# Kernel optimization log

Measured on AMD Instinct MI355X. Metric: run time of the kernel, lower is better.

The kernel has to match this reference:

```python
import jax, jax.numpy as jnp
import numpy as np

B = 16384      # batch of samples
D = 65         # inps columns: 64 input spins + 1 output spin y
NA = 64        # auxiliary (threshold) spins
N = D + NA     # spins entering vspin expansion: 129
M = N + N * (N - 1) // 2  # degree-<=2 spin monomials: 8385
GAMMA = 1.0

# pairwise index pattern (i < j), computed once at trace time
_II, _JJ = np.triu_indices(N, k=1)


def batch_vspin(b):
    # b: [B, N] -> [B, N + N(N-1)/2]: linear terms then all pairwise products b_i*b_j (i<j)
    return jnp.concatenate([b, b[:, _II] * b[:, _JJ]], axis=-1)


def setup_inputs() -> dict:
    key = jax.random.key(0)
    k1, k2, k3, k4 = jax.random.split(key, 4)
    inps = jax.random.normal(k1, (B, D), dtype=jnp.float32)
    thresh_w = jax.random.normal(k2, (NA, D), dtype=jnp.float32) * 0.1
    thresh_b = jax.random.normal(k3, (NA,), dtype=jnp.float32) * 0.1
    main_w = jax.random.normal(k4, (1, M), dtype=jnp.float32) * 0.02
    return {"inps": inps, "thresh_w": thresh_w, "thresh_b": thresh_b, "main_w": main_w}


def reference(inps, thresh_w, thresh_b, main_w):
    inps = inps.astype(jnp.float32)
    x = inps[:, :-1]                      # [B, D-1]
    y = inps[:, -1:]                      # [B, 1]
    i_right = jnp.concatenate([x, y], axis=-1)    # [B, D]
    i_wrong = jnp.concatenate([x, -y], axis=-1)   # [B, D]

    w1 = i_right @ thresh_w.T + thresh_b          # [B, NA]
    w2 = i_wrong @ thresh_w.T + thresh_b          # [B, NA]
    t1 = jnp.tanh(GAMMA * w1)
    t2 = jnp.tanh(GAMMA * w2)

    b1 = jnp.concatenate([i_right, t1], axis=-1)  # [B, N]
    b2 = jnp.concatenate([i_wrong, t2], axis=-1)  # [B, N]
    v1 = batch_vspin(b1)                          # [B, M]
    v2 = batch_vspin(b2)                          # [B, M]

    diff = (v1 - v2) @ main_w.T + 1.0             # [B, 1]
    int_penalty = jnp.sum((GAMMA / 300.0) * ((1.0 - t1 ** 2) ** 2 + (1.0 - t2 ** 2) ** 2))
    neut_penalty = jnp.sum((t2 * w2 - t1 * w1) ** 2)
    return (diff, int_penalty, neut_penalty)
```

## Files before the change

### kernel.cpp

```cpp
#include <hip/hip_runtime.h>

#define B_SZ 16384
#define N_SP 129

typedef _Float16 half8 __attribute__((ext_vector_type(8)));
typedef float float4v __attribute__((ext_vector_type(4)));

#define WS_F32_BASE 6144
#define WS_TWY  (WS_F32_BASE)
#define WS_QXY  (WS_F32_BASE + 64)
#define WS_QYT  (WS_F32_BASE + 128)
#define WS_LINT (WS_F32_BASE + 192)
#define WS_LINY (WS_F32_BASE + 256)
#define WS_P1   (WS_F32_BASE + 320)
#define WS_P2   (WS_F32_BASE + 576)

__device__ __forceinline__ int qidx(int i, int j) {
  return N_SP + i * (2 * N_SP - i - 1) / 2 + (j - i - 1);
}

__device__ __forceinline__ float fast_tanh(float x) {
  float xc = fminf(fmaxf(x, -15.f), 15.f);
  float e = __expf(2.f * xc);
  return 1.f - 2.f / (e + 1.f);
}

__global__ void setup_kernel(const float* __restrict__ mw, const float* __restrict__ tw,
                             float* __restrict__ wsf) {
  int t = blockIdx.x * blockDim.x + threadIdx.x;
  if (t < 12288) {
    int frag = t >> 9;
    int e = t & 511;
    int lane = e >> 3, j = e & 7;
    int tbl = frag >> 3;
    int tg = frag & 7;
    int kt = tg >> 2, g = tg & 3;
    int k = kt * 32 + (lane >> 4) * 8 + j;
    int n = (lane & 15) + 16 * g;
    float v;
    if (tbl == 0) {
      v = tw[n * 65 + k];
    } else if (tbl == 1) {
      v = mw[qidx(n, 65 + k)];
    } else {
      v = 0.f;
      if (n != k) {
        int a = n < k ? n : k, b = n < k ? k : n;
        v = mw[qidx(65 + a, 65 + b)];
      }
    }
    ((_Float16*)wsf)[t] = (_Float16)v;
  } else if (t < 12352) {
    int u = t - 12288; wsf[WS_TWY + u] = tw[u * 65 + 64];
  } else if (t < 12416) {
    int i = t - 12352; wsf[WS_QXY + i] = mw[qidx(i, 64)];
  } else if (t < 12480) {
    int u = t - 12416; wsf[WS_QYT + u] = mw[qidx(64, 65 + u)];
  } else if (t < 12544) {
    int u = t - 12480; wsf[WS_LINT + u] = mw[65 + u];
  } else if (t == 12544) {
    wsf[WS_LINY] = mw[64];
  }
}

__global__ void main_kernel(const float* __restrict__ inps, const float* __restrict__ tb,
                            float* __restrict__ wsf, float* __restrict__ out) {
  __shared__ __align__(16) float s_x[4 * 1056];
  __shared__ __align__(16) float s_dt[4 * 1088];
  __shared__ float s_red[8];

  const int tid = threadIdx.x;
  const int l = tid & 63, wib = tid >> 6;
  const int wave = (blockIdx.x << 2) + wib;
  const int b0 = wave << 4;
  const int q = l >> 4, m = l & 15;

  float* xw = s_x + wib * 1056;
  float* dtw = s_dt + wib * 1088;

  const float* src = inps + b0 * 65;
#pragma unroll
  for (int t = 0; t < 16; t++) xw[t * 64 + l] = src[t * 64 + l];
  if (l < 16) xw[1024 + l] = src[1024 + l];

  const half8* fragh = (const half8*)wsf;

  float twyv[4], tbv[4], qxyv[4], qytv[4], lintv[4];
#pragma unroll
  for (int g = 0; g < 4; g++) {
    int u = m + 16 * g;
    twyv[g] = wsf[WS_TWY + u];
    tbv[g] = tb[u];
    qxyv[g] = wsf[WS_QXY + u];
    qytv[g] = wsf[WS_QYT + u];
    lintv[g] = wsf[WS_LINT + u];
  }
  const float liny = wsf[WS_LINY];

  half8 ax[2];
#pragma unroll
  for (int t = 0; t < 2; t++) {
    const float* xp = xw + m * 65 + t * 32 + q * 8;
#pragma unroll
    for (int j = 0; j < 8; j++) ax[t][j] = (_Float16)xp[j];
  }

  float4v acc[4];
#pragma unroll
  for (int g = 0; g < 4; g++) { acc[g][0] = 0.f; acc[g][1] = 0.f; acc[g][2] = 0.f; acc[g][3] = 0.f; }
#pragma unroll
  for (int g = 0; g < 4; g++)
#pragma unroll
    for (int t = 0; t < 2; t++)
      acc[g] = __builtin_amdgcn_mfma_f32_16x16x32_f16(ax[t], fragh[(t * 4 + g) * 64 + l], acc[g], 0, 0, 0);

  float yv[4];
#pragma unroll
  for (int r = 0; r < 4; r++) yv[r] = xw[(q * 4 + r) * 65 + 64];
  float dtv[4][4], stv[4][4];
  float pint = 0.f, pneut = 0.f;
#pragma unroll
  for (int g = 0; g < 4; g++)
#pragma unroll
    for (int r = 0; r < 4; r++) {
      float wpre = acc[g][r] + tbv[g];
      float w1 = wpre + twyv[g] * yv[r];
      float w2 = wpre - twyv[g] * yv[r];
      float t1 = fast_tanh(w1), t2 = fast_tanh(w2);
      float dt = t1 - t2, st = t1 + t2;
      dtv[g][r] = dt; stv[g][r] = st;
      float a1 = 1.f - t1 * t1, a2 = 1.f - t2 * t2;
      pint += a1 * a1 + a2 * a2;
      float nv = t2 * w2 - t1 * w1;
      pneut += nv * nv;
      dtw[(q * 4 + r) * 68 + m + 16 * g] = dt;
    }

  half8 adt[2];
#pragma unroll
  for (int t = 0; t < 2; t++) {
    const float* dp = dtw + m * 68 + t * 32 + q * 8;
#pragma unroll
    for (int j = 0; j < 8; j++) adt[t][j] = (_Float16)dp[j];
  }

  float4v rxt[4], rtt[4];
#pragma unroll
  for (int g = 0; g < 4; g++) {
    rxt[g][0] = 0.f; rxt[g][1] = 0.f; rxt[g][2] = 0.f; rxt[g][3] = 0.f;
    rtt[g][0] = 0.f; rtt[g][1] = 0.f; rtt[g][2] = 0.f; rtt[g][3] = 0.f;
  }
#pragma unroll
  for (int g = 0; g < 4; g++)
#pragma unroll
    for (int t = 0; t < 2; t++) {
      rxt[g] = __builtin_amdgcn_mfma_f32_16x16x32_f16(adt[t], fragh[(8 + t * 4 + g) * 64 + l], rxt[g], 0, 0, 0);
      rtt[g] = __builtin_amdgcn_mfma_f32_16x16x32_f16(adt[t], fragh[(16 + t * 4 + g) * 64 + l], rtt[g], 0, 0, 0);
    }

  float creg[4] = {0.f, 0.f, 0.f, 0.f};
#pragma unroll
  for (int g = 0; g < 4; g++)
#pragma unroll
    for (int r = 0; r < 4; r++) {
      float xv = xw[(q * 4 + r) * 65 + m + 16 * g];
      creg[r] += xv * (2.f * yv[r] * qxyv[g] + rxt[g][r])
               + yv[r] * stv[g][r] * qytv[g]
               + 0.5f * stv[g][r] * rtt[g][r]
               + lintv[g] * dtv[g][r];
    }
#pragma unroll
  for (int r = 0; r < 4; r++) {
    float c = creg[r];
    c += __shfl_xor(c, 1); c += __shfl_xor(c, 2);
    c += __shfl_xor(c, 4); c += __shfl_xor(c, 8);
    if (m == 0) out[b0 + q * 4 + r] = 1.f + 2.f * yv[r] * liny + c;
  }

#pragma unroll
  for (int off = 1; off < 64; off <<= 1) {
    pint += __shfl_xor(pint, off);
    pneut += __shfl_xor(pneut, off);
  }
  if (l == 0) { s_red[wib] = pint; s_red[4 + wib] = pneut; }
  __syncthreads();
  if (tid == 0) {
    wsf[WS_P1 + blockIdx.x] = s_red[0] + s_red[1] + s_red[2] + s_red[3];
    wsf[WS_P2 + blockIdx.x] = s_red[4] + s_red[5] + s_red[6] + s_red[7];
  }
}

__global__ __launch_bounds__(256) void reduce_kernel(const float* __restrict__ wsf,
                                                     float* __restrict__ out) {
  __shared__ float s[8];
  const int tid = threadIdx.x;
  float a = wsf[WS_P1 + tid];
  float b = wsf[WS_P2 + tid];
#pragma unroll
  for (int off = 1; off < 64; off <<= 1) {
    a += __shfl_xor(a, off);
    b += __shfl_xor(b, off);
  }
  const int w = tid >> 6, l = tid & 63;
  if (l == 0) { s[w] = a; s[4 + w] = b; }
  __syncthreads();
  if (tid == 0) {
    out[B_SZ] = (s[0] + s[1] + s[2] + s[3]) * (1.f / 300.f);
    out[B_SZ + 1] = s[4] + s[5] + s[6] + s[7];
  }
}

extern "C" void kernel_launch(void* const* d_in, const int* in_sizes, int n_in,
                              void* d_out, int out_size, void* d_ws, size_t ws_size,
                              hipStream_t stream) {
  const float* inps = (const float*)d_in[0];
  const float* tw   = (const float*)d_in[1];
  const float* tb   = (const float*)d_in[2];
  const float* mw   = (const float*)d_in[3];
  float* out = (float*)d_out;
  float* wsf = (float*)d_ws;
  setup_kernel<<<50, 256, 0, stream>>>(mw, tw, wsf);
  main_kernel<<<256, 256, 0, stream>>>(inps, tb, wsf, out);
  reduce_kernel<<<1, 256, 0, stream>>>(wsf, out);
}
```

Baseline: 73.25 us.

## Fuse weight-fragment setup into main kernel via shared memory and halve rows per wave

Removes the separate setup kernel: each block now gathers the fp16 weight fragments and the small per-spin tables straight into shared memory, which saves one launch and the global workspace round-trip. The grid is doubled to 512 blocks, with each wave handling 8 samples instead of 16, so half the MFMA output rows are idle and masked. Inputs are staged as fp16 in shared memory using float4 loads, which lets fragments be read with single vector loads. The cost is that every block repeats the 12K-element weight gather from global memory, and half of the MFMA work is wasted.

```diff
diff --git a/kernel.cpp b/kernel.cpp
--- a/kernel.cpp
+++ b/kernel.cpp
@@ -2,18 +2,14 @@
 
 #define B_SZ 16384
 #define N_SP 129
+#define GRID 512
+#define BLOCK 256
 
 typedef _Float16 half8 __attribute__((ext_vector_type(8)));
 typedef float float4v __attribute__((ext_vector_type(4)));
 
-#define WS_F32_BASE 6144
-#define WS_TWY  (WS_F32_BASE)
-#define WS_QXY  (WS_F32_BASE + 64)
-#define WS_QYT  (WS_F32_BASE + 128)
-#define WS_LINT (WS_F32_BASE + 192)
-#define WS_LINY (WS_F32_BASE + 256)
-#define WS_P1   (WS_F32_BASE + 320)
-#define WS_P2   (WS_F32_BASE + 576)
+#define WS_P1 0
+#define WS_P2 512
 
 __device__ __forceinline__ int qidx(int i, int j) {
   return N_SP + i * (2 * N_SP - i - 1) / 2 + (j - i - 1);
@@ -25,15 +21,24 @@
   return 1.f - 2.f / (e + 1.f);
 }
 
-__global__ void setup_kernel(const float* __restrict__ mw, const float* __restrict__ tw,
-                             float* __restrict__ wsf) {
-  int t = blockIdx.x * blockDim.x + threadIdx.x;
-  if (t < 12288) {
-    int frag = t >> 9;
-    int e = t & 511;
+__global__ __launch_bounds__(BLOCK, 2) void main_kernel(
+    const float* __restrict__ inps, const float* __restrict__ tw,
+    const float* __restrict__ tb, const float* __restrict__ mw,
+    float* __restrict__ out, float* __restrict__ wsf) {
+  __shared__ __align__(16) _Float16 s_frag[12288];
+  __shared__ __align__(16) _Float16 s_x[4 * 1152];
+  __shared__ __align__(16) _Float16 s_dt[4 * 1152];
+  __shared__ float s_small[324];
+  __shared__ float s_red[8];
+
+  const int tid = threadIdx.x;
+
+#pragma unroll 4
+  for (int s = 0; s < 48; s++) {
+    int idx = tid + BLOCK * s;
+    int frag = idx >> 9, e = idx & 511;
     int lane = e >> 3, j = e & 7;
-    int tbl = frag >> 3;
-    int tg = frag & 7;
+    int tbl = frag >> 3, tg = frag & 7;
     int kt = tg >> 2, g = tg & 3;
     int k = kt * 32 + (lane >> 4) * 8 + j;
     int n = (lane & 15) + 16 * g;
@@ -49,61 +54,70 @@
         v = mw[qidx(65 + a, 65 + b)];
       }
     }
-    ((_Float16*)wsf)[t] = (_Float16)v;
-  } else if (t < 12352) {
-    int u = t - 12288; wsf[WS_TWY + u] = tw[u * 65 + 64];
-  } else if (t < 12416) {
-    int i = t - 12352; wsf[WS_QXY + i] = mw[qidx(i, 64)];
-  } else if (t < 12480) {
-    int u = t - 12416; wsf[WS_QYT + u] = mw[qidx(64, 65 + u)];
-  } else if (t < 12544) {
-    int u = t - 12480; wsf[WS_LINT + u] = mw[65 + u];
-  } else if (t == 12544) {
-    wsf[WS_LINY] = mw[64];
-  }
-}
-
-__global__ void main_kernel(const float* __restrict__ inps, const float* __restrict__ tb,
-                            float* __restrict__ wsf, float* __restrict__ out) {
-  __shared__ __align__(16) float s_x[4 * 1056];
-  __shared__ __align__(16) float s_dt[4 * 1088];
-  __shared__ float s_red[8];
-
-  const int tid = threadIdx.x;
+    s_frag[idx] = (_Float16)v;
+  }
+  if (tid < 64) {
+    s_small[tid]       = tw[tid * 65 + 64];
+    s_small[64 + tid]  = mw[qidx(tid, 64)];
+    s_small[128 + tid] = mw[qidx(64, 65 + tid)];
+    s_small[192 + tid] = mw[65 + tid];
+    s_small[256 + tid] = tb[tid];
+  }
+  if (tid == 0) s_small[320] = mw[64];
+
   const int l = tid & 63, wib = tid >> 6;
   const int wave = (blockIdx.x << 2) + wib;
-  const int b0 = wave << 4;
+  const int b0 = wave << 3;
+  _Float16* xw = s_x + wib * 1152;
+  _Float16* dw = s_dt + wib * 1152;
+  {
+    const float4* src4 = (const float4*)(inps + b0 * 65);
+#pragma unroll
+    for (int it = 0; it < 2; it++) {
+      float4 v = src4[l + 64 * it];
+      const float* vp = (const float*)&v;
+      int f0 = (l + 64 * it) * 4;
+#pragma unroll
+      for (int c = 0; c < 4; c++) {
+        unsigned idx = f0 + c;
+        unsigned row = idx / 65u, col = idx - row * 65u;
+        xw[row * 72 + col] = (_Float16)vp[c];
+      }
+    }
+    if (l < 2) {
+      float4 v = src4[128 + l];
+      const float* vp = (const float*)&v;
+      int f0 = (128 + l) * 4;
+#pragma unroll
+      for (int c = 0; c < 4; c++) {
+        unsigned idx = f0 + c;
+        unsigned row = idx / 65u, col = idx - row * 65u;
+        xw[row * 72 + col] = (_Float16)vp[c];
+      }
+    }
+  }
+  __syncthreads();
+
   const int q = l >> 4, m = l & 15;
-
-  float* xw = s_x + wib * 1056;
-  float* dtw = s_dt + wib * 1088;
-
-  const float* src = inps + b0 * 65;
-#pragma unroll
-  for (int t = 0; t < 16; t++) xw[t * 64 + l] = src[t * 64 + l];
-  if (l < 16) xw[1024 + l] = src[1024 + l];
-
-  const half8* fragh = (const half8*)wsf;
+  const bool act = (q < 2);
 
   float twyv[4], tbv[4], qxyv[4], qytv[4], lintv[4];
 #pragma unroll
   for (int g = 0; g < 4; g++) {
     int u = m + 16 * g;
-    twyv[g] = wsf[WS_TWY + u];
-    tbv[g] = tb[u];
-    qxyv[g] = wsf[WS_QXY + u];
-    qytv[g] = wsf[WS_QYT + u];
-    lintv[g] = wsf[WS_LINT + u];
-  }
-  const float liny = wsf[WS_LINY];
+    twyv[g] = s_small[u];
+    qxyv[g] = s_small[64 + u];
+    qytv[g] = s_small[128 + u];
+    lintv[g] = s_small[192 + u];
+    tbv[g] = s_small[256 + u];
+  }
+  const float liny = s_small[320];
+  const half8* fragv = (const half8*)s_frag;
 
   half8 ax[2];
 #pragma unroll
-  for (int t = 0; t < 2; t++) {
-    const float* xp = xw + m * 65 + t * 32 + q * 8;
-#pragma unroll
-    for (int j = 0; j < 8; j++) ax[t][j] = (_Float16)xp[j];
-  }
+  for (int t = 0; t < 2; t++)
+    ax[t] = *(const half8*)(xw + m * 72 + t * 32 + q * 8);
 
   float4v acc[4];
 #pragma unroll
@@ -112,11 +126,11 @@
   for (int g = 0; g < 4; g++)
 #pragma unroll
     for (int t = 0; t < 2; t++)
-      acc[g] = __builtin_amdgcn_mfma_f32_16x16x32_f16(ax[t], fragh[(t * 4 + g) * 64 + l], acc[g], 0, 0, 0);
+      acc[g] = __builtin_amdgcn_mfma_f32_16x16x32_f16(ax[t], fragv[(t * 4 + g) * 64 + l], acc[g], 0, 0, 0);
 
   float yv[4];
 #pragma unroll
-  for (int r = 0; r < 4; r++) yv[r] = xw[(q * 4 + r) * 65 + 64];
+  for (int r = 0; r < 4; r++) yv[r] = (float)xw[(q * 4 + r) * 72 + 64];
   float dtv[4][4], stv[4][4];
   float pint = 0.f, pneut = 0.f;
 #pragma unroll
@@ -129,20 +143,19 @@
       float t1 = fast_tanh(w1), t2 = fast_tanh(w2);
       float dt = t1 - t2, st = t1 + t2;
       dtv[g][r] = dt; stv[g][r] = st;
-      float a1 = 1.f - t1 * t1, a2 = 1.f - t2 * t2;
-      pint += a1 * a1 + a2 * a2;
-      float nv = t2 * w2 - t1 * w1;
-      pneut += nv * nv;
-      dtw[(q * 4 + r) * 68 + m + 16 * g] = dt;
+      if (act) {
+        float a1 = 1.f - t1 * t1, a2 = 1.f - t2 * t2;
+        pint += a1 * a1 + a2 * a2;
+        float nv = t2 * w2 - t1 * w1;
+        pneut += nv * nv;
+        dw[(q * 4 + r) * 72 + m + 16 * g] = (_Float16)dt;
+      }
     }
 
   half8 adt[2];
 #pragma unroll
-  for (int t = 0; t < 2; t++) {
-    const float* dp = dtw + m * 68 + t * 32 + q * 8;
-#pragma unroll
-    for (int j = 0; j < 8; j++) adt[t][j] = (_Float16)dp[j];
-  }
+  for (int t = 0; t < 2; t++)
+    adt[t] = *(const half8*)(dw + m * 72 + t * 32 + q * 8);
 
   float4v rxt[4], rtt[4];
 #pragma unroll
@@ -154,8 +167,8 @@
   for (int g = 0; g < 4; g++)
 #pragma unroll
     for (int t = 0; t < 2; t++) {
-      rxt[g] = __builtin_amdgcn_mfma_f32_16x16x32_f16(adt[t], fragh[(8 + t * 4 + g) * 64 + l], rxt[g], 0, 0, 0);
-      rtt[g] = __builtin_amdgcn_mfma_f32_16x16x32_f16(adt[t], fragh[(16 + t * 4 + g) * 64 + l], rtt[g], 0, 0, 0);
+      rxt[g] = __builtin_amdgcn_mfma_f32_16x16x32_f16(adt[t], fragv[(8 + t * 4 + g) * 64 + l], rxt[g], 0, 0, 0);
+      rtt[g] = __builtin_amdgcn_mfma_f32_16x16x32_f16(adt[t], fragv[(16 + t * 4 + g) * 64 + l], rtt[g], 0, 0, 0);
     }
 
   float creg[4] = {0.f, 0.f, 0.f, 0.f};
@@ -163,7 +176,7 @@
   for (int g = 0; g < 4; g++)
 #pragma unroll
     for (int r = 0; r < 4; r++) {
-      float xv = xw[(q * 4 + r) * 65 + m + 16 * g];
+      float xv = (float)xw[(q * 4 + r) * 72 + m + 16 * g];
       creg[r] += xv * (2.f * yv[r] * qxyv[g] + rxt[g][r])
                + yv[r] * stv[g][r] * qytv[g]
                + 0.5f * stv[g][r] * rtt[g][r]
@@ -174,7 +187,7 @@
     float c = creg[r];
     c += __shfl_xor(c, 1); c += __shfl_xor(c, 2);
     c += __shfl_xor(c, 4); c += __shfl_xor(c, 8);
-    if (m == 0) out[b0 + q * 4 + r] = 1.f + 2.f * yv[r] * liny + c;
+    if (act && m == 0) out[b0 + q * 4 + r] = 1.f + 2.f * yv[r] * liny + c;
   }
 
 #pragma unroll
@@ -190,9 +203,9 @@
   }
 }
 
-__global__ __launch_bounds__(256) void reduce_kernel(const float* __restrict__ wsf,
+__global__ __launch_bounds__(512) void reduce_kernel(const float* __restrict__ wsf,
                                                      float* __restrict__ out) {
-  __shared__ float s[8];
+  __shared__ float s[16];
   const int tid = threadIdx.x;
   float a = wsf[WS_P1 + tid];
   float b = wsf[WS_P2 + tid];
@@ -202,11 +215,14 @@
     b += __shfl_xor(b, off);
   }
   const int w = tid >> 6, l = tid & 63;
-  if (l == 0) { s[w] = a; s[4 + w] = b; }
+  if (l == 0) { s[w] = a; s[8 + w] = b; }
   __syncthreads();
   if (tid == 0) {
-    out[B_SZ] = (s[0] + s[1] + s[2] + s[3]) * (1.f / 300.f);
-    out[B_SZ + 1] = s[4] + s[5] + s[6] + s[7];
+    float sa = 0.f, sb = 0.f;
+#pragma unroll
+    for (int i = 0; i < 8; i++) { sa += s[i]; sb += s[8 + i]; }
+    out[B_SZ] = sa * (1.f / 300.f);
+    out[B_SZ + 1] = sb;
   }
 }
 
@@ -219,7 +235,6 @@
   const float* mw   = (const float*)d_in[3];
   float* out = (float*)d_out;
   float* wsf = (float*)d_ws;
-  setup_kernel<<<50, 256, 0, stream>>>(mw, tw, wsf);
-  main_kernel<<<256, 256, 0, stream>>>(inps, tb, wsf, out);
-  reduce_kernel<<<1, 256, 0, stream>>>(wsf, out);
-}
+  main_kernel<<<GRID, BLOCK, 0, stream>>>(inps, tw, tb, mw, out, wsf);
+  reduce_kernel<<<1, 512, 0, stream>>>(wsf, out);
+}
```

Result: slower. 83.32 us (+13.8%).

## Halve rows per wave, use fp16 LDS staging, atomic penalty reduction

Applied to the files above, without the earlier changes.

Each wave now handles 8 samples instead of 16 (the 16-row MFMA tile is half-filled), and the grid doubles to 512 blocks for more parallelism. Inputs are loaded with float4 and staged in LDS as fp16 with padded rows, so MFMA operands can be read as single half8 vector loads. Weight fragments are preloaded into registers. The separate reduce kernel is replaced by per-wave atomicAdds into the output, with zeroing done in setup. This trades wasted MFMA lanes and atomic contention for fewer kernel launches and more concurrent waves.

```diff
diff --git a/kernel.cpp b/kernel.cpp
--- a/kernel.cpp
+++ b/kernel.cpp
@@ -2,6 +2,8 @@
 
 #define B_SZ 16384
 #define N_SP 129
+#define GRID 512
+#define BLOCK 256
 
 typedef _Float16 half8 __attribute__((ext_vector_type(8)));
 typedef float float4v __attribute__((ext_vector_type(4)));
@@ -12,8 +14,6 @@
 #define WS_QYT  (WS_F32_BASE + 128)
 #define WS_LINT (WS_F32_BASE + 192)
 #define WS_LINY (WS_F32_BASE + 256)
-#define WS_P1   (WS_F32_BASE + 320)
-#define WS_P2   (WS_F32_BASE + 576)
 
 __device__ __forceinline__ int qidx(int i, int j) {
   return N_SP + i * (2 * N_SP - i - 1) / 2 + (j - i - 1);
@@ -26,14 +26,13 @@
 }
 
 __global__ void setup_kernel(const float* __restrict__ mw, const float* __restrict__ tw,
-                             float* __restrict__ wsf) {
+                             float* __restrict__ wsf, float* __restrict__ out) {
   int t = blockIdx.x * blockDim.x + threadIdx.x;
+  if (t == 0) { out[B_SZ] = 0.f; out[B_SZ + 1] = 0.f; }
   if (t < 12288) {
-    int frag = t >> 9;
-    int e = t & 511;
+    int frag = t >> 9, e = t & 511;
     int lane = e >> 3, j = e & 7;
-    int tbl = frag >> 3;
-    int tg = frag & 7;
+    int tbl = frag >> 3, tg = frag & 7;
     int kt = tg >> 2, g = tg & 3;
     int k = kt * 32 + (lane >> 4) * 8 + j;
     int n = (lane & 15) + 16 * g;
@@ -63,47 +62,74 @@
   }
 }
 
-__global__ void main_kernel(const float* __restrict__ inps, const float* __restrict__ tb,
-                            float* __restrict__ wsf, float* __restrict__ out) {
-  __shared__ __align__(16) float s_x[4 * 1056];
-  __shared__ __align__(16) float s_dt[4 * 1088];
-  __shared__ float s_red[8];
+__global__ __launch_bounds__(BLOCK, 2) void main_kernel(
+    const float* __restrict__ inps, const float* __restrict__ tb,
+    const float* __restrict__ wsf, float* __restrict__ out) {
+  __shared__ __align__(16) _Float16 s_x[4 * 1152];
+  __shared__ __align__(16) _Float16 s_dt[4 * 1152];
 
   const int tid = threadIdx.x;
   const int l = tid & 63, wib = tid >> 6;
   const int wave = (blockIdx.x << 2) + wib;
-  const int b0 = wave << 4;
+  const int b0 = wave << 3;
   const int q = l >> 4, m = l & 15;
-
-  float* xw = s_x + wib * 1056;
-  float* dtw = s_dt + wib * 1088;
-
-  const float* src = inps + b0 * 65;
-#pragma unroll
-  for (int t = 0; t < 16; t++) xw[t * 64 + l] = src[t * 64 + l];
-  if (l < 16) xw[1024 + l] = src[1024 + l];
-
-  const half8* fragh = (const half8*)wsf;
-
+  const bool act = (q < 2);
+
+  _Float16* xw = s_x + wib * 1152;
+  _Float16* dw = s_dt + wib * 1152;
+
+  const half8* fragv = (const half8*)wsf;
+  half8 f_tw[8], f_qxt[8], f_qtt[8];
+#pragma unroll
+  for (int f = 0; f < 8; f++) {
+    f_tw[f]  = fragv[f * 64 + l];
+    f_qxt[f] = fragv[(8 + f) * 64 + l];
+    f_qtt[f] = fragv[(16 + f) * 64 + l];
+  }
   float twyv[4], tbv[4], qxyv[4], qytv[4], lintv[4];
 #pragma unroll
   for (int g = 0; g < 4; g++) {
     int u = m + 16 * g;
     twyv[g] = wsf[WS_TWY + u];
-    tbv[g] = tb[u];
     qxyv[g] = wsf[WS_QXY + u];
     qytv[g] = wsf[WS_QYT + u];
     lintv[g] = wsf[WS_LINT + u];
+    tbv[g] = tb[u];
   }
   const float liny = wsf[WS_LINY];
 
+  {
+    const float4* src4 = (const float4*)(inps + b0 * 65);
+    float4 v0 = src4[l];
+    float4 v1 = src4[64 + l];
+#pragma unroll
+    for (int c = 0; c < 4; c++) {
+      unsigned idx = l * 4 + c;
+      unsigned row = idx / 65u, col = idx - row * 65u;
+      xw[row * 72 + col] = (_Float16)((const float*)&v0)[c];
+    }
+#pragma unroll
+    for (int c = 0; c < 4; c++) {
+      unsigned idx = (64 + l) * 4 + c;
+      unsigned row = idx / 65u, col = idx - row * 65u;
+      xw[row * 72 + col] = (_Float16)((const float*)&v1)[c];
+    }
+    if (l < 2) {
+      float4 v2 = src4[128 + l];
+#pragma unroll
+      for (int c = 0; c < 4; c++) {
+        unsigned idx = (128 + l) * 4 + c;
+        unsigned row = idx / 65u, col = idx - row * 65u;
+        xw[row * 72 + col] = (_Float16)((const float*)&v2)[c];
+      }
+    }
+  }
+  __syncthreads();
+
   half8 ax[2];
 #pragma unroll
-  for (int t = 0; t < 2; t++) {
-    const float* xp = xw + m * 65 + t * 32 + q * 8;
-#pragma unroll
-    for (int j = 0; j < 8; j++) ax[t][j] = (_Float16)xp[j];
-  }
+  for (int t = 0; t < 2; t++)
+    ax[t] = *(const half8*)(xw + m * 72 + t * 32 + q * 8);
 
   float4v acc[4];
 #pragma unroll
@@ -112,11 +138,11 @@
   for (int g = 0; g < 4; g++)
 #pragma unroll
     for (int t = 0; t < 2; t++)
-      acc[g] = __builtin_amdgcn_mfma_f32_16x16x32_f16(ax[t], fragh[(t * 4 + g) * 64 + l], acc[g], 0, 0, 0);
+      acc[g] = __builtin_amdgcn_mfma_f32_16x16x32_f16(ax[t], f_tw[t * 4 + g], acc[g], 0, 0, 0);
 
   float yv[4];
 #pragma unroll
-  for (int r = 0; r < 4; r++) yv[r] = xw[(q * 4 + r) * 65 + 64];
+  for (int r = 0; r < 4; r++) yv[r] = (float)xw[(q * 4 + r) * 72 + 64];
   float dtv[4][4], stv[4][4];
   float pint = 0.f, pneut = 0.f;
 #pragma unroll
@@ -129,20 +155,19 @@
       float t1 = fast_tanh(w1), t2 = fast_tanh(w2);
       float dt = t1 - t2, st = t1 + t2;
       dtv[g][r] = dt; stv[g][r] = st;
-      float a1 = 1.f - t1 * t1, a2 = 1.f - t2 * t2;
-      pint += a1 * a1 + a2 * a2;
-      float nv = t2 * w2 - t1 * w1;
-      pneut += nv * nv;
-      dtw[(q * 4 + r) * 68 + m + 16 * g] = dt;
+      if (act) {
+        float a1 = 1.f - t1 * t1, a2 = 1.f - t2 * t2;
+        pint += a1 * a1 + a2 * a2;
+        float nv = t2 * w2 - t1 * w1;
+        pneut += nv * nv;
+        dw[(q * 4 + r) * 72 + m + 16 * g] = (_Float16)dt;
+      }
     }
 
   half8 adt[2];
 #pragma unroll
-  for (int t = 0; t < 2; t++) {
-    const float* dp = dtw + m * 68 + t * 32 + q * 8;
-#pragma unroll
-    for (int j = 0; j < 8; j++) adt[t][j] = (_Float16)dp[j];
-  }
+  for (int t = 0; t < 2; t++)
+    adt[t] = *(const half8*)(dw + m * 72 + t * 32 + q * 8);
 
   float4v rxt[4], rtt[4];
 #pragma unroll
@@ -154,8 +179,8 @@
   for (int g = 0; g < 4; g++)
 #pragma unroll
     for (int t = 0; t < 2; t++) {
-      rxt[g] = __builtin_amdgcn_mfma_f32_16x16x32_f16(adt[t], fragh[(8 + t * 4 + g) * 64 + l], rxt[g], 0, 0, 0);
-      rtt[g] = __builtin_amdgcn_mfma_f32_16x16x32_f16(adt[t], fragh[(16 + t * 4 + g) * 64 + l], rtt[g], 0, 0, 0);
+      rxt[g] = __builtin_amdgcn_mfma_f32_16x16x32_f16(adt[t], f_qxt[t * 4 + g], rxt[g], 0, 0, 0);
+      rtt[g] = __builtin_amdgcn_mfma_f32_16x16x32_f16(adt[t], f_qtt[t * 4 + g], rtt[g], 0, 0, 0);
     }
 
   float creg[4] = {0.f, 0.f, 0.f, 0.f};
@@ -163,7 +188,7 @@
   for (int g = 0; g < 4; g++)
 #pragma unroll
     for (int r = 0; r < 4; r++) {
-      float xv = xw[(q * 4 + r) * 65 + m + 16 * g];
+      float xv = (float)xw[(q * 4 + r) * 72 + m + 16 * g];
       creg[r] += xv * (2.f * yv[r] * qxyv[g] + rxt[g][r])
                + yv[r] * stv[g][r] * qytv[g]
                + 0.5f * stv[g][r] * rtt[g][r]
@@ -174,7 +199,7 @@
     float c = creg[r];
     c += __shfl_xor(c, 1); c += __shfl_xor(c, 2);
     c += __shfl_xor(c, 4); c += __shfl_xor(c, 8);
-    if (m == 0) out[b0 + q * 4 + r] = 1.f + 2.f * yv[r] * liny + c;
+    if (act && m == 0) out[b0 + q * 4 + r] = 1.f + 2.f * yv[r] * liny + c;
   }
 
 #pragma unroll
@@ -182,31 +207,9 @@
     pint += __shfl_xor(pint, off);
     pneut += __shfl_xor(pneut, off);
   }
-  if (l == 0) { s_red[wib] = pint; s_red[4 + wib] = pneut; }
-  __syncthreads();
-  if (tid == 0) {
-    wsf[WS_P1 + blockIdx.x] = s_red[0] + s_red[1] + s_red[2] + s_red[3];
-    wsf[WS_P2 + blockIdx.x] = s_red[4] + s_red[5] + s_red[6] + s_red[7];
-  }
-}
-
-__global__ __launch_bounds__(256) void reduce_kernel(const float* __restrict__ wsf,
-                                                     float* __restrict__ out) {
-  __shared__ float s[8];
-  const int tid = threadIdx.x;
-  float a = wsf[WS_P1 + tid];
-  float b = wsf[WS_P2 + tid];
-#pragma unroll
-  for (int off = 1; off < 64; off <<= 1) {
-    a += __shfl_xor(a, off);
-    b += __shfl_xor(b, off);
-  }
-  const int w = tid >> 6, l = tid & 63;
-  if (l == 0) { s[w] = a; s[4 + w] = b; }
-  __syncthreads();
-  if (tid == 0) {
-    out[B_SZ] = (s[0] + s[1] + s[2] + s[3]) * (1.f / 300.f);
-    out[B_SZ + 1] = s[4] + s[5] + s[6] + s[7];
+  if (l == 0) {
+    atomicAdd(&out[B_SZ], pint * (1.f / 300.f));
+    atomicAdd(&out[B_SZ + 1], pneut);
   }
 }
 
@@ -219,7 +222,6 @@
   const float* mw   = (const float*)d_in[3];
   float* out = (float*)d_out;
   float* wsf = (float*)d_ws;
-  setup_kernel<<<50, 256, 0, stream>>>(mw, tw, wsf);
-  main_kernel<<<256, 256, 0, stream>>>(inps, tb, wsf, out);
-  reduce_kernel<<<1, 256, 0, stream>>>(wsf, out);
-}
+  setup_kernel<<<50, 256, 0, stream>>>(mw, tw, wsf, out);
+  main_kernel<<<GRID, BLOCK, 0, stream>>>(inps, tb, wsf, out);
+}
```

Result: slower. 120.7 us (+64.8%).
